# Kernel tuning notes

Measured on AMD Instinct MI355X. Metric: run time of the kernel, lower is better.

Reference implementation:

```python
import jax, jax.numpy as jnp
import numpy as np


def _gru_scan(xg, w_hh, b_hh, h0):
    """Scan a GRU (PyTorch gate order r,z,n) over time. xg: (T,B,3H) precomputed input projections."""
    def step(h, g):
        gh = h @ w_hh.T + b_hh
        i_r, i_z, i_n = jnp.split(g, 3, axis=-1)
        h_r, h_z, h_n = jnp.split(gh, 3, axis=-1)
        r = jax.nn.sigmoid(i_r + h_r)
        z = jax.nn.sigmoid(i_z + h_z)
        n = jnp.tanh(i_n + r * h_n)
        h_new = (1.0 - z) * n + z * h
        return h_new, h_new
    _, ys = jax.lax.scan(step, h0, xg)
    return ys  # (T, B, H)


def setup_inputs() -> dict:
    key = jax.random.key(0)
    ks = jax.random.split(key, 13)
    B, M, T = 64, 80, 2000
    C, H, K = 256, 256, 5
    s = 0.1
    return {
        "x": jax.random.normal(ks[0], (B, M, T), jnp.float32),
        "conv_w": jax.random.normal(ks[1], (C, M, K), jnp.float32) * s,
        "conv_b": jax.random.normal(ks[2], (C,), jnp.float32) * s,
        "w_ih_f": jax.random.normal(ks[3], (3 * H, C), jnp.float32) * s,
        "w_hh_f": jax.random.normal(ks[4], (3 * H, H), jnp.float32) * s,
        "b_ih_f": jax.random.normal(ks[5], (3 * H,), jnp.float32) * s,
        "b_hh_f": jax.random.normal(ks[6], (3 * H,), jnp.float32) * s,
        "w_ih_r": jax.random.normal(ks[7], (3 * H, C), jnp.float32) * s,
        "w_hh_r": jax.random.normal(ks[8], (3 * H, H), jnp.float32) * s,
        "b_ih_r": jax.random.normal(ks[9], (3 * H,), jnp.float32) * s,
        "b_hh_r": jax.random.normal(ks[10], (3 * H,), jnp.float32) * s,
        "clf_w": jax.random.normal(ks[11], (2, 2 * H), jnp.float32) * s,
        "clf_b": jax.random.normal(ks[12], (2,), jnp.float32) * s,
        "window_size": 100,
    }


def reference(x, conv_w, conv_b, w_ih_f, w_hh_f, b_ih_f, b_hh_f,
              w_ih_r, w_hh_r, b_ih_r, b_hh_r, clf_w, clf_b, window_size):
    # Streaming (inference_mode) branch of KWSNet, expressed incrementally:
    # per-step sliding-window conv == full valid conv; the 'bidirectional' GRU
    # with seq_len=1 per step and carried hidden == two independent GRUs both
    # scanned forward in time (one with the _reverse weight set).
    B = x.shape[0]
    K = conv_w.shape[-1]
    H = w_hh_f.shape[-1]
    # Conv1d valid + ReLU: (B, C, Tc), Tc = T - K + 1
    y = jax.lax.conv_general_dilated(x, conv_w, (1,), 'VALID',
                                     dimension_numbers=('NCH', 'OIH', 'NCH'))
    y = jax.nn.relu(y + conv_b[None, :, None])
    seq = jnp.transpose(y, (2, 0, 1))  # (Tc, B, C)
    h0 = jnp.zeros((B, H), seq.dtype)
    xg_f = seq @ w_ih_f.T + b_ih_f  # (Tc, B, 3H)
    xg_r = seq @ w_ih_r.T + b_ih_r
    enc = jnp.concatenate([
        _gru_scan(xg_f, w_hh_f, b_hh_f, h0),
        _gru_scan(xg_r, w_hh_r, b_hh_r, h0),
    ], axis=-1)  # (Tc, B, 2H)
    # Sliding mean over the last W encoder outputs (W = window_size - K + 1)
    W = window_size - K + 1
    cs = jnp.concatenate([jnp.zeros_like(enc[:1]), jnp.cumsum(enc, axis=0)], axis=0)
    means = (cs[W:] - cs[:-W]) / W  # (Tout, B, 2H), Tout = T - window_size + 1
    out = means @ clf_w.T + clf_b  # (Tout, B, 2)
    # torch stacks per-step (1, B, 2) outputs -> (Tout, 1, B, 2)
    return out[:, None, :, :]
```

## Files before the change

### kernel.cpp

```cpp
#include <hip/hip_runtime.h>
#include <hip/hip_bf16.h>


#define TT    2000
#define TC    1996
#define NB    64
#define MCH   80
#define NN    1536
#define TOUT  1901
#define TCH   126
#define NCHK  16
#define CROWS (TCH * NB)

typedef _Float16 h8_t __attribute__((ext_vector_type(8)));
typedef float    f4_t __attribute__((ext_vector_type(4)));

#define WQSCALE 254.0f
#define INV8    (1.0f / (254.0f * 127.0f))

#define OFF_SEQC ((size_t)0)
#define OFF_XG   ((size_t)8257536)
#define OFF_WT   ((size_t)57802752)
#define OFF_WCAT ((size_t)58212352)
#define OFF_HST  ((size_t)58998784)
#define OFF_WQ   ((size_t)59129856)
#define OFF_PS2  ((size_t)59523072)

__global__ void prep_kernel(const float* __restrict__ conv_w,
                            const float* __restrict__ wihf,
                            const float* __restrict__ wihr,
                            const float* __restrict__ whhf,
                            const float* __restrict__ whhr,
                            float* __restrict__ wT,
                            _Float16* __restrict__ wcat,
                            unsigned* __restrict__ wq) {
    int idx = blockIdx.x * 256 + threadIdx.x;
    if (idx < 400 * 256) {
        int c = idx & 255, mk = idx >> 8;
        wT[idx] = conv_w[c * 400 + mk];
    }
    int i2 = idx - 400 * 256;
    if (i2 >= 0 && i2 < NN * 256) {
        int k = i2 & 255, n = i2 >> 8;
        float v = (n < 768) ? wihf[n * 256 + k] : wihr[(n - 768) * 256 + k];
        wcat[i2] = (_Float16)v;
    }
    int i4 = idx - (400 * 256 + NN * 256);
    if (i4 >= 0 && i4 < 2 * 3 * 256 * 64) {
        int r  = i4 & 255;
        int j  = (i4 >> 8) & 63;
        int dg = i4 >> 14;
        const float* whh = (dg >= 3) ? whhr : whhf;
        int g = (dg >= 3) ? dg - 3 : dg;
        const float* wp = whh + (size_t)(g * 256 + r) * 256 + 4 * j;
        unsigned v = 0;
#pragma unroll
        for (int kk = 0; kk < 4; ++kk) {
            float q = rintf(wp[kk] * WQSCALE);
            q = fminf(fmaxf(q, -127.f), 127.f);
            v |= ((unsigned)((int)q & 0xFF)) << (8 * kk);
        }
        wq[((size_t)dg * 256 + r) * 64 + j] = v;
    }
}

#define SD4(a, b, c) __builtin_amdgcn_sdot4((int)(a), (int)(b), (c), false)

__global__ __launch_bounds__(256)
void fat_kernel(
    int nscan, const _Float16* __restrict__ xg_s, const uint4* __restrict__ wq,
    const float* __restrict__ bhhf, const float* __restrict__ bhhr,
    const float* __restrict__ clfw, float* __restrict__ hstate,
    float* __restrict__ psum2, int t0s, int lens, int first,
    int nproj, const _Float16* __restrict__ seqc_p, const _Float16* __restrict__ wcat,
    const float* __restrict__ bihf, const float* __restrict__ bihr,
    _Float16* __restrict__ xg_p,
    int nconv, const float* __restrict__ x, const float* __restrict__ wT,
    const float* __restrict__ conv_b, _Float16* __restrict__ seqc_c,
    int t0c, int lenc)
{
    __shared__ __align__(16) char smem[86016];
    int bid = blockIdx.x;
    int tid = threadIdx.x;

    if (bid < nscan) {
        int d = bid >> 6, b = bid & 63;
        int i = tid, lane = tid & 63, wv = tid >> 6;
        const float* bhh = d ? bhhr : bhhf;
        unsigned (*hq8)[64]  = (unsigned(*)[64])smem;
        float (*cwp)[4][2]   = (float(*)[4][2])(smem + 512);

        uint4 wa[16], wb[16], wc[16];
        {
            const uint4* pa = wq + ((size_t)(d * 3 + 0) * 256 + i) * 16;
            const uint4* pb = wq + ((size_t)(d * 3 + 1) * 256 + i) * 16;
            const uint4* pc = wq + ((size_t)(d * 3 + 2) * 256 + i) * 16;
#pragma unroll
            for (int k = 0; k < 16; ++k) { wa[k] = pa[k]; wb[k] = pb[k]; wc[k] = pc[k]; }
        }
        float bhr = bhh[i], bhz = bhh[256 + i], bhn = bhh[512 + i];
        float cw0 = clfw[d * 256 + i], cw1 = clfw[512 + d * 256 + i];
        float h = first ? 0.f : hstate[(size_t)bid * 256 + i];

        ((char*)&hq8[0][0])[i] = (char)(int)rintf(h * 127.f);
        __syncthreads();

        const _Float16* xgp = xg_s + (size_t)d * CROWS * 768 + (size_t)b * 768 + i;
        float xr = (float)xgp[0], xz = (float)xgp[256], xn = (float)xgp[512];
        xgp += (size_t)64 * 768;

        int cur = 0;
        for (int t = 0; t < lens; ++t) {
            float pxr = (float)xgp[0], pxz = (float)xgp[256], pxn = (float)xgp[512];
            xgp += (size_t)64 * 768;

            const uint4* hqp = (const uint4*)&hq8[cur][0];
            int i0 = 0, i1 = 0, i2 = 0;
#pragma unroll
            for (int k = 0; k < 16; ++k) {
                uint4 hv = hqp[k];
                i0 = SD4(wa[k].x, hv.x, i0); i0 = SD4(wa[k].y, hv.y, i0);
                i0 = SD4(wa[k].z, hv.z, i0); i0 = SD4(wa[k].w, hv.w, i0);
                i1 = SD4(wb[k].x, hv.x, i1); i1 = SD4(wb[k].y, hv.y, i1);
                i1 = SD4(wb[k].z, hv.z, i1); i1 = SD4(wb[k].w, hv.w, i1);
                i2 = SD4(wc[k].x, hv.x, i2); i2 = SD4(wc[k].y, hv.y, i2);
                i2 = SD4(wc[k].z, hv.z, i2); i2 = SD4(wc[k].w, hv.w, i2);
            }

            float hr = (float)i0 * INV8 + bhr;
            float hz = (float)i1 * INV8 + bhz;
            float hn = (float)i2 * INV8 + bhn;
            float rg = 1.f / (1.f + __expf(-(xr + hr)));
            float zg = 1.f / (1.f + __expf(-(xz + hz)));
            float xnr = xn + rg * hn;
            float nv = 1.f - 2.f / (__expf(2.f * xnr) + 1.f);
            h = (1.f - zg) * nv + zg * h;

            float s0 = cw0 * h, s1 = cw1 * h;
#pragma unroll
            for (int off = 32; off; off >>= 1) {
                s0 += __shfl_xor(s0, off, 64);
                s1 += __shfl_xor(s1, off, 64);
            }
            int nxt = cur ^ 1;
            ((char*)&hq8[nxt][0])[i] = (char)(int)rintf(h * 127.f);
            if (lane == 0) { cwp[nxt][wv][0] = s0; cwp[nxt][wv][1] = s1; }
            __syncthreads();
            if (i == 0) {
                float a0 = cwp[nxt][0][0] + cwp[nxt][1][0] + cwp[nxt][2][0] + cwp[nxt][3][0];
                float a1 = cwp[nxt][0][1] + cwp[nxt][1][1] + cwp[nxt][2][1] + cwp[nxt][3][1];
                float* pp = psum2 + (((size_t)d * TC + (t0s + t)) * 64 + b) * 2;
                pp[0] = a0; pp[1] = a1;
            }
            cur = nxt;
            xr = pxr; xz = pxz; xn = pxn;
        }
        hstate[(size_t)bid * 256 + i] = h;

    } else if (bid < nscan + nproj) {
        int pb = bid - nscan;
        int row0 = (pb / 12) * 128;
        int n0   = (pb % 12) * 128;
        _Float16 (*As)[72] = (_Float16(*)[72])smem;
        _Float16 (*Bs)[72] = (_Float16(*)[72])(smem + 18432);
        int lane = tid & 63, wv = tid >> 6;
        int wr = wv >> 1, wcn = wv & 1;
        int fm = lane & 15, fq = lane >> 4;
        f4_t acc[4][4];
#pragma unroll
        for (int mt = 0; mt < 4; ++mt)
#pragma unroll
            for (int nt = 0; nt < 4; ++nt) acc[mt][nt] = (f4_t){0.f, 0.f, 0.f, 0.f};

        int r = tid >> 1, part = tid & 1;
        for (int kc = 0; kc < 4; ++kc) {
            const uint4* srcA = (const uint4*)&seqc_p[(size_t)(row0 + r) * 256 + kc * 64 + part * 32];
            const uint4* srcB = (const uint4*)&wcat[(size_t)(n0 + r) * 256 + kc * 64 + part * 32];
            uint4* dstA = (uint4*)&As[r][part * 32];
            uint4* dstB = (uint4*)&Bs[r][part * 32];
            dstA[0] = srcA[0]; dstA[1] = srcA[1]; dstA[2] = srcA[2]; dstA[3] = srcA[3];
            dstB[0] = srcB[0]; dstB[1] = srcB[1]; dstB[2] = srcB[2]; dstB[3] = srcB[3];
            __syncthreads();
#pragma unroll
            for (int ks = 0; ks < 64; ks += 32) {
                h8_t af[4], bf[4];
#pragma unroll
                for (int mt = 0; mt < 4; ++mt)
                    af[mt] = *(const h8_t*)&As[wr * 64 + mt * 16 + fm][ks + fq * 8];
#pragma unroll
                for (int nt = 0; nt < 4; ++nt)
                    bf[nt] = *(const h8_t*)&Bs[wcn * 64 + nt * 16 + fm][ks + fq * 8];
#pragma unroll
                for (int mt = 0; mt < 4; ++mt)
#pragma unroll
                    for (int nt = 0; nt < 4; ++nt)
                        acc[mt][nt] = __builtin_amdgcn_mfma_f32_16x16x32_f16(
                            af[mt], bf[nt], acc[mt][nt], 0, 0, 0);
            }
            __syncthreads();
        }
#pragma unroll
        for (int nt = 0; nt < 4; ++nt) {
            int col = n0 + wcn * 64 + nt * 16 + fm;
            int d = (col < 768) ? 0 : 1;
            int j = col - d * 768;
            float bias = d ? bihr[j] : bihf[j];
            size_t obase = (size_t)d * CROWS * 768 + j;
#pragma unroll
            for (int mt = 0; mt < 4; ++mt) {
                int row = row0 + wr * 64 + mt * 16 + fq * 4;
#pragma unroll
                for (int rr = 0; rr < 4; ++rr)
                    xg_p[obase + (size_t)(row + rr) * 768] = (_Float16)(acc[mt][nt][rr] + bias);
            }
        }

    } else {
        int cb = bid - nscan - nproj;
        int tile = cb >> 6;
        int b    = cb & 63;
        float (*xs)[68] = (float(*)[68])smem;
        for (int idx = tid; idx < MCH * 68; idx += 256) {
            int m = idx / 68, ii = idx - m * 68;
            int tt = t0c + tile * 64 + ii;
            xs[m][ii] = (tt < TT) ? x[(size_t)b * (MCH * TT) + m * TT + tt] : 0.f;
        }
        __syncthreads();
        int lane = tid & 63, tg = tid >> 6;
        float acc[4][16];
#pragma unroll
        for (int cq = 0; cq < 4; ++cq)
#pragma unroll
            for (int t = 0; t < 16; ++t) acc[cq][t] = 0.f;

        for (int m = 0; m < MCH; ++m) {
            float xr_[20];
#pragma unroll
            for (int q = 0; q < 5; ++q) {
                float4 v = *(const float4*)&xs[m][tg * 16 + q * 4];
                xr_[q * 4 + 0] = v.x; xr_[q * 4 + 1] = v.y;
                xr_[q * 4 + 2] = v.z; xr_[q * 4 + 3] = v.w;
            }
#pragma unroll
            for (int cq = 0; cq < 4; ++cq) {
                int c = lane + cq * 64;
                const float* wp = wT + (size_t)(m * 5) * 256 + c;
                float w0_ = wp[0], w1_ = wp[256], w2_ = wp[512], w3_ = wp[768], w4_ = wp[1024];
#pragma unroll
                for (int t = 0; t < 16; ++t)
                    acc[cq][t] += w0_ * xr_[t] + w1_ * xr_[t + 1] + w2_ * xr_[t + 2]
                                + w3_ * xr_[t + 3] + w4_ * xr_[t + 4];
            }
        }
#pragma unroll
        for (int cq = 0; cq < 4; ++cq) {
            int c = lane + cq * 64;
            float cb_ = conv_b[c];
            for (int t = 0; t < 16; ++t) {
                int tl = tile * 64 + tg * 16 + t;
                if (tl < lenc) {
                    float v = acc[cq][t] + cb_;
                    v = v > 0.f ? v : 0.f;
                    seqc_c[((size_t)tl * 64 + b) * 256 + c] = (_Float16)v;
                }
            }
        }
    }
}

__global__ void final_kernel(const float* __restrict__ psum2, const float* __restrict__ clf_b,
                             const int* __restrict__ win, float* __restrict__ out) {
    int idx = blockIdx.x * 256 + threadIdx.x;
    if (idx >= TOUT * 128) return;
    int c = idx & 1;
    int rem = idx >> 1;
    int b = rem & 63;
    int tau = rem >> 6;
    int W = win[0] - 5 + 1;
    const float* p0 = psum2;
    const float* p1 = psum2 + (size_t)TC * 64 * 2;
    float s = 0.f;
    for (int j = 0; j < W; ++j) {
        size_t o = ((size_t)(tau + j) * 64 + b) * 2 + c;
        s += p0[o] + p1[o];
    }
    out[idx] = s / (float)W + clf_b[c];
}

extern "C" void kernel_launch(void* const* d_in, const int* in_sizes, int n_in,
                              void* d_out, int out_size, void* d_ws, size_t ws_size,
                              hipStream_t stream) {
    const float* x      = (const float*)d_in[0];
    const float* conv_w = (const float*)d_in[1];
    const float* conv_b = (const float*)d_in[2];
    const float* w_ih_f = (const float*)d_in[3];
    const float* w_hh_f = (const float*)d_in[4];
    const float* b_ih_f = (const float*)d_in[5];
    const float* b_hh_f = (const float*)d_in[6];
    const float* w_ih_r = (const float*)d_in[7];
    const float* w_hh_r = (const float*)d_in[8];
    const float* b_ih_r = (const float*)d_in[9];
    const float* b_hh_r = (const float*)d_in[10];
    const float* clf_w  = (const float*)d_in[11];
    const float* clf_b  = (const float*)d_in[12];
    const int*   win    = (const int*)d_in[13];
    float* out = (float*)d_out;

    char* ws = (char*)d_ws;
    _Float16* seqc = (_Float16*)(ws + OFF_SEQC);
    _Float16* xg   = (_Float16*)(ws + OFF_XG);
    float*    wT   = (float*)(ws + OFF_WT);
    _Float16* wcat = (_Float16*)(ws + OFF_WCAT);
    float*    hst  = (float*)(ws + OFF_HST);
    const uint4* wqp = (const uint4*)(ws + OFF_WQ);
    unsigned* wq   = (unsigned*)(ws + OFF_WQ);
    float*    ps2  = (float*)(ws + OFF_PS2);

    const size_t XGP = (size_t)2 * CROWS * 768;
    const size_t SQP = (size_t)CROWS * 256;

    int prep_elems = 400 * 256 + NN * 256 + 2 * 3 * 256 * 64;
    prep_kernel<<<(prep_elems + 255) / 256, 256, 0, stream>>>(
        conv_w, w_ih_f, w_ih_r, w_hh_f, w_hh_r, wT, wcat, wq);

    auto lenk = [](int k) { return (k < NCHK - 1) ? TCH : (TC - (NCHK - 1) * TCH); };

    fat_kernel<<<128, 256, 0, stream>>>(
        0, xg, wqp, b_hh_f, b_hh_r, clf_w, hst, ps2, 0, 0, 0,
        0, seqc, wcat, b_ih_f, b_ih_r, xg,
        128, x, wT, conv_b, seqc, 0, lenk(0));

    fat_kernel<<<(lenk(0) / 2) * 12 + 128, 256, 0, stream>>>(
        0, xg, wqp, b_hh_f, b_hh_r, clf_w, hst, ps2, 0, 0, 0,
        (lenk(0) / 2) * 12, seqc, wcat, b_ih_f, b_ih_r, xg,
        128, x, wT, conv_b, seqc + SQP, TCH, lenk(1));

    for (int k = 0; k < NCHK; ++k) {
        int lens = lenk(k);
        int np = (k + 1 < NCHK) ? (lenk(k + 1) / 2) * 12 : 0;
        int nc = (k + 2 < NCHK) ? 128 : 0;
        fat_kernel<<<128 + np + nc, 256, 0, stream>>>(
            128, xg + (size_t)(k & 1) * XGP, wqp, b_hh_f, b_hh_r, clf_w, hst, ps2,
            k * TCH, lens, (k == 0) ? 1 : 0,
            np, seqc + (size_t)((k + 1) & 1) * SQP, wcat, b_ih_f, b_ih_r,
            xg + (size_t)((k + 1) & 1) * XGP,
            nc, x, wT, conv_b, seqc + (size_t)(k & 1) * SQP,
            (k + 2) * TCH, (k + 2 < NCHK) ? lenk(k + 2) : 0);
    }

    final_kernel<<<(TOUT * 128 + 255) / 256, 256, 0, stream>>>(ps2, clf_b, win, out);
}
```

Baseline: 2.371 ms.

## Make projection blocks persistent with full weight slab resident in LDS

Projection GEMM blocks now load their full 128x256 weight column slab into shared memory once, then loop over row tiles with a stride of NRG. The launch uses 12*NRG projection blocks instead of one block per tile. This removes repeated weight loads per tile and cuts block count, so fewer projection blocks compete with the latency-critical scan blocks. It uses more shared memory per block and gives each block serialized work.

```diff
diff --git a/kernel.cpp b/kernel.cpp
--- a/kernel.cpp
+++ b/kernel.cpp
@@ -10,6 +10,7 @@
 #define TOUT  1901
 #define TCH   126
 #define NCHK  16
+#define NRG   9
 #define CROWS (TCH * NB)
 
 typedef _Float16 h8_t __attribute__((ext_vector_type(8)));
@@ -74,7 +75,7 @@
     float* __restrict__ psum2, int t0s, int lens, int first,
     int nproj, const _Float16* __restrict__ seqc_p, const _Float16* __restrict__ wcat,
     const float* __restrict__ bihf, const float* __restrict__ bihr,
-    _Float16* __restrict__ xg_p,
+    _Float16* __restrict__ xg_p, int lenp,
     int nconv, const float* __restrict__ x, const float* __restrict__ wT,
     const float* __restrict__ conv_b, _Float16* __restrict__ seqc_c,
     int t0c, int lenc)
@@ -159,59 +160,68 @@
 
     } else if (bid < nscan + nproj) {
         int pb = bid - nscan;
-        int row0 = (pb / 12) * 128;
-        int n0   = (pb % 12) * 128;
-        _Float16 (*As)[72] = (_Float16(*)[72])smem;
-        _Float16 (*Bs)[72] = (_Float16(*)[72])(smem + 18432);
+        int n0 = (pb % 12) * 128;
+        int rg = pb / 12;
+        int ntiles = lenp >> 1;
+        _Float16 (*Bs)[264] = (_Float16(*)[264])smem;
+        _Float16 (*As)[72]  = (_Float16(*)[72])(smem + 67584);
         int lane = tid & 63, wv = tid >> 6;
         int wr = wv >> 1, wcn = wv & 1;
         int fm = lane & 15, fq = lane >> 4;
-        f4_t acc[4][4];
-#pragma unroll
-        for (int mt = 0; mt < 4; ++mt)
-#pragma unroll
-            for (int nt = 0; nt < 4; ++nt) acc[mt][nt] = (f4_t){0.f, 0.f, 0.f, 0.f};
-
         int r = tid >> 1, part = tid & 1;
-        for (int kc = 0; kc < 4; ++kc) {
-            const uint4* srcA = (const uint4*)&seqc_p[(size_t)(row0 + r) * 256 + kc * 64 + part * 32];
-            const uint4* srcB = (const uint4*)&wcat[(size_t)(n0 + r) * 256 + kc * 64 + part * 32];
-            uint4* dstA = (uint4*)&As[r][part * 32];
-            uint4* dstB = (uint4*)&Bs[r][part * 32];
-            dstA[0] = srcA[0]; dstA[1] = srcA[1]; dstA[2] = srcA[2]; dstA[3] = srcA[3];
-            dstB[0] = srcB[0]; dstB[1] = srcB[1]; dstB[2] = srcB[2]; dstB[3] = srcB[3];
-            __syncthreads();
-#pragma unroll
-            for (int ks = 0; ks < 64; ks += 32) {
-                h8_t af[4], bf[4];
-#pragma unroll
-                for (int mt = 0; mt < 4; ++mt)
-                    af[mt] = *(const h8_t*)&As[wr * 64 + mt * 16 + fm][ks + fq * 8];
-#pragma unroll
-                for (int nt = 0; nt < 4; ++nt)
-                    bf[nt] = *(const h8_t*)&Bs[wcn * 64 + nt * 16 + fm][ks + fq * 8];
-#pragma unroll
-                for (int mt = 0; mt < 4; ++mt)
+
+        {
+            const uint4* srcB = (const uint4*)&wcat[(size_t)(n0 + r) * 256 + part * 128];
+            uint4* dstB = (uint4*)&Bs[r][part * 128];
+#pragma unroll
+            for (int q = 0; q < 16; ++q) dstB[q] = srcB[q];
+        }
+
+        for (int tIdx = rg; tIdx < ntiles; tIdx += NRG) {
+            int row0 = tIdx * 128;
+            f4_t acc[4][4];
+#pragma unroll
+            for (int mt = 0; mt < 4; ++mt)
+#pragma unroll
+                for (int nt = 0; nt < 4; ++nt) acc[mt][nt] = (f4_t){0.f, 0.f, 0.f, 0.f};
+
+            for (int kc = 0; kc < 4; ++kc) {
+                const uint4* srcA = (const uint4*)&seqc_p[(size_t)(row0 + r) * 256 + kc * 64 + part * 32];
+                uint4* dstA = (uint4*)&As[r][part * 32];
+                dstA[0] = srcA[0]; dstA[1] = srcA[1]; dstA[2] = srcA[2]; dstA[3] = srcA[3];
+                __syncthreads();
+#pragma unroll
+                for (int ks = 0; ks < 64; ks += 32) {
+                    h8_t af[4], bf[4];
+#pragma unroll
+                    for (int mt = 0; mt < 4; ++mt)
+                        af[mt] = *(const h8_t*)&As[wr * 64 + mt * 16 + fm][ks + fq * 8];
 #pragma unroll
                     for (int nt = 0; nt < 4; ++nt)
-                        acc[mt][nt] = __builtin_amdgcn_mfma_f32_16x16x32_f16(
-                            af[mt], bf[nt], acc[mt][nt], 0, 0, 0);
-            }
-            __syncthreads();
-        }
-#pragma unroll
-        for (int nt = 0; nt < 4; ++nt) {
-            int col = n0 + wcn * 64 + nt * 16 + fm;
-            int d = (col < 768) ? 0 : 1;
-            int j = col - d * 768;
-            float bias = d ? bihr[j] : bihf[j];
-            size_t obase = (size_t)d * CROWS * 768 + j;
-#pragma unroll
-            for (int mt = 0; mt < 4; ++mt) {
-                int row = row0 + wr * 64 + mt * 16 + fq * 4;
-#pragma unroll
-                for (int rr = 0; rr < 4; ++rr)
-                    xg_p[obase + (size_t)(row + rr) * 768] = (_Float16)(acc[mt][nt][rr] + bias);
+                        bf[nt] = *(const h8_t*)&Bs[wcn * 64 + nt * 16 + fm][kc * 64 + ks + fq * 8];
+#pragma unroll
+                    for (int mt = 0; mt < 4; ++mt)
+#pragma unroll
+                        for (int nt = 0; nt < 4; ++nt)
+                            acc[mt][nt] = __builtin_amdgcn_mfma_f32_16x16x32_f16(
+                                af[mt], bf[nt], acc[mt][nt], 0, 0, 0);
+                }
+                __syncthreads();
+            }
+#pragma unroll
+            for (int nt = 0; nt < 4; ++nt) {
+                int col = n0 + wcn * 64 + nt * 16 + fm;
+                int d = (col < 768) ? 0 : 1;
+                int j = col - d * 768;
+                float bias = d ? bihr[j] : bihf[j];
+                size_t obase = (size_t)d * CROWS * 768 + j;
+#pragma unroll
+                for (int mt = 0; mt < 4; ++mt) {
+                    int row = row0 + wr * 64 + mt * 16 + fq * 4;
+#pragma unroll
+                    for (int rr = 0; rr < 4; ++rr)
+                        xg_p[obase + (size_t)(row + rr) * 768] = (_Float16)(acc[mt][nt][rr] + bias);
+                }
             }
         }
 
@@ -327,23 +337,24 @@
 
     fat_kernel<<<128, 256, 0, stream>>>(
         0, xg, wqp, b_hh_f, b_hh_r, clf_w, hst, ps2, 0, 0, 0,
-        0, seqc, wcat, b_ih_f, b_ih_r, xg,
+        0, seqc, wcat, b_ih_f, b_ih_r, xg, 0,
         128, x, wT, conv_b, seqc, 0, lenk(0));
 
-    fat_kernel<<<(lenk(0) / 2) * 12 + 128, 256, 0, stream>>>(
+    fat_kernel<<<12 * NRG + 128, 256, 0, stream>>>(
         0, xg, wqp, b_hh_f, b_hh_r, clf_w, hst, ps2, 0, 0, 0,
-        (lenk(0) / 2) * 12, seqc, wcat, b_ih_f, b_ih_r, xg,
+        12 * NRG, seqc, wcat, b_ih_f, b_ih_r, xg, lenk(0),
         128, x, wT, conv_b, seqc + SQP, TCH, lenk(1));
 
     for (int k = 0; k < NCHK; ++k) {
         int lens = lenk(k);
-        int np = (k + 1 < NCHK) ? (lenk(k + 1) / 2) * 12 : 0;
+        int np = (k + 1 < NCHK) ? 12 * NRG : 0;
+        int lp = (k + 1 < NCHK) ? lenk(k + 1) : 0;
         int nc = (k + 2 < NCHK) ? 128 : 0;
         fat_kernel<<<128 + np + nc, 256, 0, stream>>>(
             128, xg + (size_t)(k & 1) * XGP, wqp, b_hh_f, b_hh_r, clf_w, hst, ps2,
             k * TCH, lens, (k == 0) ? 1 : 0,
             np, seqc + (size_t)((k + 1) & 1) * SQP, wcat, b_ih_f, b_ih_r,
-            xg + (size_t)((k + 1) & 1) * XGP,
+            xg + (size_t)((k + 1) & 1) * XGP, lp,
             nc, x, wT, conv_b, seqc + (size_t)(k & 1) * SQP,
             (k + 2) * TCH, (k + 2 < NCHK) ? lenk(k + 2) : 0);
     }
```

Measured after the change: 2.363 ms, median of 2. About the same (-0.3%).
